# Kernel tuning notes

Hardware: AMD Instinct MI355X
Metric: run time of the kernel (lower is better)

Reference implementation:

```python
import jax, jax.numpy as jnp
import numpy as np

WH, WW = 8, 8
N = WH * WW
DIM = 128
H = 4
B_ = 8192


def _make_buffers():
    # relative_coords_table: [1, 2Wh-1, 2Ww-1, 2]
    ch = np.arange(-(WH - 1), WH, dtype=np.float32)
    cw = np.arange(-(WW - 1), WW, dtype=np.float32)
    gh, gw = np.meshgrid(ch, cw, indexing='ij')
    table = np.stack([gh, gw], axis=-1)[None]  # [1, 2Wh-1, 2Ww-1, 2]
    table[..., 0] /= (WH - 1 + 1e-12)
    table[..., 1] /= (WW - 1 + 1e-12)
    table *= 8.0
    table = np.sign(table) * np.log2(np.abs(table) + 1.0) / np.log2(8.0)
    # relative_position_index: [N, N]
    yh, yw = np.meshgrid(np.arange(WH), np.arange(WW), indexing='ij')
    coords = np.stack([yh, yw]).reshape(2, -1)  # [2, N]
    rel = coords[:, :, None] - coords[:, None, :]  # [2, N, N]
    rel = rel.transpose(1, 2, 0).astype(np.int64)
    rel[..., 0] += WH - 1
    rel[..., 1] += WW - 1
    rel[..., 0] *= 2 * WW - 1
    idx = rel.sum(-1)
    return jnp.asarray(table, jnp.float32), jnp.asarray(idx, jnp.int32)


def setup_inputs() -> dict:
    key = jax.random.key(0)
    ks = jax.random.split(key, 9)
    s = 0.02
    rel_table, rel_index = _make_buffers()
    return {
        'x': jax.random.normal(ks[0], (B_, N, DIM), jnp.float32),
        'W_qkv': jax.random.normal(ks[1], (3 * DIM, DIM), jnp.float32) * s,
        'q_bias': jax.random.normal(ks[2], (DIM,), jnp.float32) * s,
        'v_bias': jax.random.normal(ks[3], (DIM,), jnp.float32) * s,
        'logit_scale': jnp.full((H, 1, 1), jnp.log(10.0), jnp.float32),
        'cpb_w1': jax.random.normal(ks[4], (512, 2), jnp.float32) * s,
        'cpb_b1': jax.random.normal(ks[5], (512,), jnp.float32) * s,
        'cpb_w2': jax.random.normal(ks[6], (H, 512), jnp.float32) * s,
        'proj_w': jax.random.normal(ks[7], (DIM, DIM), jnp.float32) * s,
        'proj_b': jax.random.normal(ks[8], (DIM,), jnp.float32) * s,
        'rel_table': rel_table,
        'rel_index': rel_index,
    }


def reference(x, W_qkv, q_bias, v_bias, logit_scale, cpb_w1, cpb_b1, cpb_w2,
              proj_w, proj_b, rel_table, rel_index):
    B, n, C = x.shape
    hd = C // H
    # qkv projection with Swin-V2 bias layout (k bias frozen at zero)
    qkv_bias = jnp.concatenate([q_bias, jnp.zeros_like(v_bias), v_bias])
    qkv = x @ W_qkv.T + qkv_bias               # [B, N, 3C]
    qkv = qkv.reshape(B, n, 3, H, hd).transpose(2, 0, 3, 1, 4)
    q, k, v = qkv[0], qkv[1], qkv[2]           # [B, H, N, hd]
    # cosine attention
    qn = q / jnp.maximum(jnp.linalg.norm(q, axis=-1, keepdims=True), 1e-12)
    kn = k / jnp.maximum(jnp.linalg.norm(k, axis=-1, keepdims=True), 1e-12)
    attn = jnp.einsum('bhnd,bhmd->bhnm', qn, kn)
    scale = jnp.exp(jnp.minimum(logit_scale, jnp.log(1.0 / 0.01)))  # [H,1,1]
    attn = attn * scale
    # continuous position bias MLP -> gather -> 16*sigmoid
    hmid = jax.nn.relu(rel_table @ cpb_w1.T + cpb_b1)      # [1,15,15,512]
    bias_table = (hmid @ cpb_w2.T).reshape(-1, H)          # [(2Wh-1)(2Ww-1), H]
    rpb = bias_table[rel_index.reshape(-1)].reshape(n, n, H)
    rpb = 16.0 * jax.nn.sigmoid(rpb.transpose(2, 0, 1))    # [H, N, N]
    attn = jax.nn.softmax(attn + rpb[None], axis=-1)
    out = jnp.einsum('bhnm,bhmd->bhnd', attn, v)           # [B, H, N, hd]
    out = out.transpose(0, 2, 1, 3).reshape(B, n, C)
    return out @ proj_w.T + proj_b
```

## Files before the change

kernel.cpp:

```cpp
#include <hip/hip_runtime.h>

typedef short bf16x8 __attribute__((ext_vector_type(8)));
typedef float f32x4 __attribute__((ext_vector_type(4)));

__device__ __forceinline__ unsigned cvt_pk_bf16(float lo, float hi) {
  unsigned r;
  asm("v_cvt_pk_bf16_f32 %0, %1, %2" : "=v"(r) : "v"(lo), "v"(hi));
  return r;
}

__device__ __forceinline__ bf16x8 pack4(unsigned a, unsigned b, unsigned c, unsigned d) {
  union { unsigned u[4]; bf16x8 v; } t;
  t.u[0] = a; t.u[1] = b; t.u[2] = c; t.u[3] = d;
  return t.v;
}

__device__ __forceinline__ unsigned short f2bf(float f) {
  unsigned u = __float_as_uint(f);
  unsigned r = (u + 0x7fffu + ((u >> 16) & 1u)) >> 16;
  return (unsigned short)r;
}

__global__ __launch_bounds__(256) void prep(
    const float* __restrict__ W_qkv, const float* __restrict__ proj_w,
    const float* __restrict__ cpb_w1, const float* __restrict__ cpb_b1,
    const float* __restrict__ cpb_w2, const float* __restrict__ rel_table,
    const int* __restrict__ rel_index,
    bf16x8* __restrict__ wq, bf16x8* __restrict__ wp, float* __restrict__ rpbf)
{
  const int b = blockIdx.x, t = threadIdx.x;
  if (b < 32) {
    int g = b * 256 + t;
    if (g < 6144) {
      int c = g >> 8, kk = (g >> 6) & 3, l = g & 63;
      const float* s = W_qkv + (c * 16 + (l & 15)) * 128 + kk * 32 + (l >> 4) * 8;
      bf16x8 v;
      #pragma unroll
      for (int j = 0; j < 8; ++j) v[j] = (short)f2bf(s[j]);
      wq[g] = v;
    } else {
      int gl = g - 6144;
      int c = gl >> 8, kk = (gl >> 6) & 3, l = gl & 63;
      const float* row = proj_w + (c * 16 + (l & 15)) * 128;
      bf16x8 v;
      #pragma unroll
      for (int j = 0; j < 8; ++j)
        v[j] = (short)f2bf(row[kk * 32 + (j >> 2) * 16 + (l >> 4) * 4 + (j & 3)]);
      wp[gl] = v;
    }
  } else {
    __shared__ float bt[900];
    if (t < 225) {
      float t0 = rel_table[t * 2], t1 = rel_table[t * 2 + 1];
      float a0 = 0.f, a1 = 0.f, a2 = 0.f, a3 = 0.f;
      for (int j = 0; j < 512; ++j) {
        float hm = fmaxf(t0 * cpb_w1[j * 2] + t1 * cpb_w1[j * 2 + 1] + cpb_b1[j], 0.f);
        a0 += hm * cpb_w2[j];
        a1 += hm * cpb_w2[512 + j];
        a2 += hm * cpb_w2[1024 + j];
        a3 += hm * cpb_w2[1536 + j];
      }
      bt[t * 4 + 0] = a0; bt[t * 4 + 1] = a1;
      bt[t * 4 + 2] = a2; bt[t * 4 + 3] = a3;
    }
    __syncthreads();
    for (int i = t; i < 16384; i += 256) {
      int hrc = i >> 8, lane = (i >> 2) & 63, j = i & 3;
      int hh = hrc >> 4, r = (hrc >> 2) & 3, c = hrc & 3;
      int n = r * 16 + (lane & 15);
      int m = c * 16 + ((lane >> 4) << 2) + j;
      float v = bt[rel_index[n * 64 + m] * 4 + hh];
      rpbf[i] = 16.0f * __fdividef(1.0f, 1.0f + __expf(-v));
    }
  }
}

__global__ __launch_bounds__(256, 3) void win_attn(
    const float* __restrict__ x,
    const float* __restrict__ q_bias,
    const float* __restrict__ v_bias,
    const float* __restrict__ logit_scale,
    const float* __restrict__ proj_b,
    const float* __restrict__ rpbf,
    const bf16x8* __restrict__ wq,
    const bf16x8* __restrict__ wp,
    float* __restrict__ out)
{
  __shared__ __align__(128) char lds[16384];
  const int tid  = threadIdx.x;
  const int lane = tid & 63;
  const int h    = tid >> 6;
  const int l15  = lane & 15;
  const int l4   = lane >> 4;
  const int swl  = (l15 & 7) << 4;
  const long base = (long)blockIdx.x * 8192;
  const f32x4 fzero = {0.f, 0.f, 0.f, 0.f};

  {
    const float4* xp = (const float4*)(x + base);
    #pragma unroll
    for (int i = 0; i < 8; ++i) {
      float4 v = xp[i * 256 + tid];
      int e   = (i * 256 + tid) * 4;
      int row = e >> 7;
      int cb  = (e & 127) * 2;
      uint2 pk = { cvt_pk_bf16(v.x, v.y), cvt_pk_bf16(v.z, v.w) };
      *(uint2*)(lds + ((row * 256 + cb) ^ ((row & 7) << 4))) = pk;
    }
  }
  __syncthreads();

  bf16x8 aq[4], bk[4], bv[2][2];

  {
    f32x4 qT[2][4], kT[2][4];
    #pragma unroll
    for (int ct = 0; ct < 2; ++ct)
      #pragma unroll
      for (int rt = 0; rt < 4; ++rt) { qT[ct][rt] = fzero; kT[ct][rt] = fzero; }

    #pragma unroll
    for (int kk = 0; kk < 4; ++kk) {
      bf16x8 a[4];
      #pragma unroll
      for (int rt = 0; rt < 4; ++rt) {
        int row = rt * 16 + l15;
        a[rt] = *(const bf16x8*)(lds + ((row * 256 + kk * 64 + l4 * 16) ^ swl));
      }
      #pragma unroll
      for (int ct = 0; ct < 2; ++ct) {
        bf16x8 wqf = wq[((2 * h + ct) * 4 + kk) * 64 + lane];
        bf16x8 wkf = wq[((8 + 2 * h + ct) * 4 + kk) * 64 + lane];
        #pragma unroll
        for (int rt = 0; rt < 4; ++rt) {
          qT[ct][rt] = __builtin_amdgcn_mfma_f32_16x16x32_bf16(wqf, a[rt], qT[ct][rt], 0, 0, 0);
          kT[ct][rt] = __builtin_amdgcn_mfma_f32_16x16x32_bf16(wkf, a[rt], kT[ct][rt], 0, 0, 0);
        }
      }
    }

    float scale = __expf(fminf(logit_scale[h], 4.6051701859880914f));
    float4 qb0 = *(const float4*)&q_bias[h * 32 + l4 * 4];
    float4 qb1 = *(const float4*)&q_bias[h * 32 + 16 + l4 * 4];
    #pragma unroll
    for (int rt = 0; rt < 4; ++rt) {
      float tq0 = qT[0][rt][0] + qb0.x, tq1 = qT[0][rt][1] + qb0.y;
      float tq2 = qT[0][rt][2] + qb0.z, tq3 = qT[0][rt][3] + qb0.w;
      float tq4 = qT[1][rt][0] + qb1.x, tq5 = qT[1][rt][1] + qb1.y;
      float tq6 = qT[1][rt][2] + qb1.z, tq7 = qT[1][rt][3] + qb1.w;
      float sq = tq0*tq0 + tq1*tq1 + tq2*tq2 + tq3*tq3
               + tq4*tq4 + tq5*tq5 + tq6*tq6 + tq7*tq7;
      float sk = kT[0][rt][0]*kT[0][rt][0] + kT[0][rt][1]*kT[0][rt][1]
               + kT[0][rt][2]*kT[0][rt][2] + kT[0][rt][3]*kT[0][rt][3]
               + kT[1][rt][0]*kT[1][rt][0] + kT[1][rt][1]*kT[1][rt][1]
               + kT[1][rt][2]*kT[1][rt][2] + kT[1][rt][3]*kT[1][rt][3];
      sq += __shfl_xor(sq, 16); sq += __shfl_xor(sq, 32);
      sk += __shfl_xor(sk, 16); sk += __shfl_xor(sk, 32);
      float iq = __fdividef(scale, fmaxf(sqrtf(sq), 1e-12f));
      float ik = __fdividef(1.0f,  fmaxf(sqrtf(sk), 1e-12f));
      aq[rt] = pack4(cvt_pk_bf16(tq0 * iq, tq1 * iq), cvt_pk_bf16(tq2 * iq, tq3 * iq),
                     cvt_pk_bf16(tq4 * iq, tq5 * iq), cvt_pk_bf16(tq6 * iq, tq7 * iq));
      bk[rt] = pack4(cvt_pk_bf16(kT[0][rt][0] * ik, kT[0][rt][1] * ik),
                     cvt_pk_bf16(kT[0][rt][2] * ik, kT[0][rt][3] * ik),
                     cvt_pk_bf16(kT[1][rt][0] * ik, kT[1][rt][1] * ik),
                     cvt_pk_bf16(kT[1][rt][2] * ik, kT[1][rt][3] * ik));
    }
  }

  {
    f32x4 vN[2][4];
    #pragma unroll
    for (int ct = 0; ct < 2; ++ct)
      #pragma unroll
      for (int rt = 0; rt < 4; ++rt) vN[ct][rt] = fzero;

    #pragma unroll
    for (int kk = 0; kk < 4; ++kk) {
      bf16x8 a[4];
      #pragma unroll
      for (int rt = 0; rt < 4; ++rt) {
        int row = rt * 16 + l15;
        a[rt] = *(const bf16x8*)(lds + ((row * 256 + kk * 64 + l4 * 16) ^ swl));
      }
      #pragma unroll
      for (int ct = 0; ct < 2; ++ct) {
        bf16x8 wvf = wq[((16 + 2 * h + ct) * 4 + kk) * 64 + lane];
        #pragma unroll
        for (int rt = 0; rt < 4; ++rt)
          vN[ct][rt] = __builtin_amdgcn_mfma_f32_16x16x32_bf16(a[rt], wvf, vN[ct][rt], 0, 0, 0);
      }
    }
    __syncthreads();

    float vb0 = v_bias[h * 32 + l15], vb1 = v_bias[h * 32 + 16 + l15];
    #pragma unroll
    for (int ks = 0; ks < 2; ++ks)
      #pragma unroll
      for (int ct = 0; ct < 2; ++ct) {
        float vb = ct ? vb1 : vb0;
        bv[ks][ct] = pack4(
            cvt_pk_bf16(vN[ct][2 * ks][0] + vb, vN[ct][2 * ks][1] + vb),
            cvt_pk_bf16(vN[ct][2 * ks][2] + vb, vN[ct][2 * ks][3] + vb),
            cvt_pk_bf16(vN[ct][2 * ks + 1][0] + vb, vN[ct][2 * ks + 1][1] + vb),
            cvt_pk_bf16(vN[ct][2 * ks + 1][2] + vb, vN[ct][2 * ks + 1][3] + vb));
      }
  }

  {
    const f32x4* rp = (const f32x4*)rpbf;
    #pragma unroll
    for (int r = 0; r < 4; ++r) {
      f32x4 st[4];
      #pragma unroll
      for (int c = 0; c < 4; ++c)
        st[c] = __builtin_amdgcn_mfma_f32_16x16x32_bf16(
            bk[c], aq[r], rp[(h * 16 + r * 4 + c) * 64 + lane], 0, 0, 0);

      float mx = st[0][0];
      #pragma unroll
      for (int c = 0; c < 4; ++c)
        #pragma unroll
        for (int j = 0; j < 4; ++j) mx = fmaxf(mx, st[c][j]);
      mx = fmaxf(mx, __shfl_xor(mx, 16));
      mx = fmaxf(mx, __shfl_xor(mx, 32));

      float e[4][4];
      float sum = 0.f;
      #pragma unroll
      for (int c = 0; c < 4; ++c)
        #pragma unroll
        for (int j = 0; j < 4; ++j) { e[c][j] = __expf(st[c][j] - mx); sum += e[c][j]; }
      sum += __shfl_xor(sum, 16); sum += __shfl_xor(sum, 32);
      float rs = __fdividef(1.0f, sum);

      bf16x8 ap0 = pack4(cvt_pk_bf16(e[0][0], e[0][1]), cvt_pk_bf16(e[0][2], e[0][3]),
                         cvt_pk_bf16(e[1][0], e[1][1]), cvt_pk_bf16(e[1][2], e[1][3]));
      bf16x8 ap1 = pack4(cvt_pk_bf16(e[2][0], e[2][1]), cvt_pk_bf16(e[2][2], e[2][3]),
                         cvt_pk_bf16(e[3][0], e[3][1]), cvt_pk_bf16(e[3][2], e[3][3]));

      f32x4 o0 = __builtin_amdgcn_mfma_f32_16x16x32_bf16(bv[0][0], ap0, fzero, 0, 0, 0);
      o0 = __builtin_amdgcn_mfma_f32_16x16x32_bf16(bv[1][0], ap1, o0, 0, 0, 0);
      f32x4 o1 = __builtin_amdgcn_mfma_f32_16x16x32_bf16(bv[0][1], ap0, fzero, 0, 0, 0);
      o1 = __builtin_amdgcn_mfma_f32_16x16x32_bf16(bv[1][1], ap1, o1, 0, 0, 0);

      int n = r * 16 + l15;
      uint4 w = { cvt_pk_bf16(o0[0] * rs, o0[1] * rs), cvt_pk_bf16(o0[2] * rs, o0[3] * rs),
                  cvt_pk_bf16(o1[0] * rs, o1[1] * rs), cvt_pk_bf16(o1[2] * rs, o1[3] * rs) };
      *(uint4*)(lds + ((n * 256 + h * 64 + 16 * l4) ^ ((n & 7) << 4))) = w;
    }
  }
  __syncthreads();

  {
    const int n = h * 16 + l15;
    f32x4 po[8];
    #pragma unroll
    for (int c2 = 0; c2 < 8; ++c2) po[c2] = fzero;
    #pragma unroll
    for (int kk = 0; kk < 4; ++kk) {
      bf16x8 ob = *(const bf16x8*)(lds + ((n * 256 + kk * 64 + 16 * l4) ^ swl));
      #pragma unroll
      for (int c2 = 0; c2 < 8; ++c2) {
        bf16x8 wf = wp[(c2 * 4 + kk) * 64 + lane];
        po[c2] = __builtin_amdgcn_mfma_f32_16x16x32_bf16(wf, ob, po[c2], 0, 0, 0);
      }
    }
    float* op = out + base + (long)n * 128;
    #pragma unroll
    for (int c2 = 0; c2 < 8; ++c2) {
      float4 pb = *(const float4*)&proj_b[c2 * 16 + l4 * 4];
      float4 v = { po[c2][0] + pb.x, po[c2][1] + pb.y,
                   po[c2][2] + pb.z, po[c2][3] + pb.w };
      *(float4*)&op[c2 * 16 + l4 * 4] = v;
    }
  }
}

extern "C" void kernel_launch(void* const* d_in, const int* in_sizes, int n_in,
                              void* d_out, int out_size, void* d_ws, size_t ws_size,
                              hipStream_t stream) {
  (void)n_in; (void)out_size; (void)ws_size;
  const float* x           = (const float*)d_in[0];
  const float* W_qkv       = (const float*)d_in[1];
  const float* q_bias      = (const float*)d_in[2];
  const float* v_bias      = (const float*)d_in[3];
  const float* logit_scale = (const float*)d_in[4];
  const float* cpb_w1      = (const float*)d_in[5];
  const float* cpb_b1      = (const float*)d_in[6];
  const float* cpb_w2      = (const float*)d_in[7];
  const float* proj_w      = (const float*)d_in[8];
  const float* proj_b      = (const float*)d_in[9];
  const float* rel_table   = (const float*)d_in[10];
  const int*   rel_index   = (const int*)d_in[11];

  float*  rpbf = (float*)d_ws;
  bf16x8* wq   = (bf16x8*)((char*)d_ws + 65536);
  bf16x8* wp   = (bf16x8*)((char*)d_ws + 65536 + 98304);

  int nwin = in_sizes[0] / 8192;

  prep<<<33, 256, 0, stream>>>(W_qkv, proj_w, cpb_w1, cpb_b1, cpb_w2,
                               rel_table, rel_index, wq, wp, rpbf);
  win_attn<<<nwin, 256, 0, stream>>>(x, q_bias, v_bias, logit_scale, proj_b,
                                     rpbf, wq, wp, (float*)d_out);
}
```

Baseline: 246.0 us.

## Make window-attention kernel persistent over 8 windows with register prefetch of next x

Each block now processes 8 windows in a loop instead of one, prefetching the next window's x into registers during the projection epilogue and alternating between two LDS buffers. Barriers become a raw lgkmcnt wait plus s_barrier, the occupancy hint rises from 3 to 4 blocks, and output stores become nontemporal. The aim is to hide global load latency and amortise per-block launch and weight-fetch overhead. The cost is 1024 blocks instead of 8192, which may leave the GPU less balanced, plus extra register pressure from the prefetch buffer.

```diff
diff --git a/kernel.cpp b/kernel.cpp
--- a/kernel.cpp
+++ b/kernel.cpp
@@ -1,4 +1,6 @@
 #include <hip/hip_runtime.h>
+
+#define WPB 8
 
 typedef short bf16x8 __attribute__((ext_vector_type(8)));
 typedef float f32x4 __attribute__((ext_vector_type(4)));
@@ -19,6 +21,10 @@
   unsigned u = __float_as_uint(f);
   unsigned r = (u + 0x7fffu + ((u >> 16) & 1u)) >> 16;
   return (unsigned short)r;
+}
+
+__device__ __forceinline__ void bar_lds() {
+  asm volatile("s_waitcnt lgkmcnt(0)\n\ts_barrier" ::: "memory");
 }
 
 __global__ __launch_bounds__(256) void prep(
@@ -75,7 +81,7 @@
   }
 }
 
-__global__ __launch_bounds__(256, 3) void win_attn(
+__global__ __launch_bounds__(256, 4) void win_attn(
     const float* __restrict__ x,
     const float* __restrict__ q_bias,
     const float* __restrict__ v_bias,
@@ -84,194 +90,217 @@
     const float* __restrict__ rpbf,
     const bf16x8* __restrict__ wq,
     const bf16x8* __restrict__ wp,
-    float* __restrict__ out)
+    float* __restrict__ out, int nwin)
 {
-  __shared__ __align__(128) char lds[16384];
+  __shared__ __align__(128) char lds[2][16384];
   const int tid  = threadIdx.x;
   const int lane = tid & 63;
   const int h    = tid >> 6;
   const int l15  = lane & 15;
   const int l4   = lane >> 4;
   const int swl  = (l15 & 7) << 4;
-  const long base = (long)blockIdx.x * 8192;
   const f32x4 fzero = {0.f, 0.f, 0.f, 0.f};
 
+  const int w0 = blockIdx.x * WPB;
+  const int rem = nwin - w0;
+  const int nw = rem < WPB ? rem : WPB;
+
+  float4 pf[8];
   {
-    const float4* xp = (const float4*)(x + base);
+    const float4* xp = (const float4*)(x + (long)w0 * 8192);
+    #pragma unroll
+    for (int i = 0; i < 8; ++i) pf[i] = xp[i * 256 + tid];
+  }
+
+  for (int w = 0; w < nw; ++w) {
+    char* buf = lds[w & 1];
+    const long base = (long)(w0 + w) * 8192;
+
+    const bf16x8* wql = wq;                 asm("" : "+s"(wql));
+    const bf16x8* wpl = wp;                 asm("" : "+s"(wpl));
+    const f32x4*  rp  = (const f32x4*)rpbf; asm("" : "+s"(rp));
+
     #pragma unroll
     for (int i = 0; i < 8; ++i) {
-      float4 v = xp[i * 256 + tid];
+      float4 v = pf[i];
       int e   = (i * 256 + tid) * 4;
       int row = e >> 7;
       int cb  = (e & 127) * 2;
       uint2 pk = { cvt_pk_bf16(v.x, v.y), cvt_pk_bf16(v.z, v.w) };
-      *(uint2*)(lds + ((row * 256 + cb) ^ ((row & 7) << 4))) = pk;
-    }
-  }
-  __syncthreads();
-
-  bf16x8 aq[4], bk[4], bv[2][2];
-
-  {
-    f32x4 qT[2][4], kT[2][4];
-    #pragma unroll
-    for (int ct = 0; ct < 2; ++ct)
-      #pragma unroll
-      for (int rt = 0; rt < 4; ++rt) { qT[ct][rt] = fzero; kT[ct][rt] = fzero; }
-
-    #pragma unroll
-    for (int kk = 0; kk < 4; ++kk) {
-      bf16x8 a[4];
+      *(uint2*)(buf + ((row * 256 + cb) ^ ((row & 7) << 4))) = pk;
+    }
+    bar_lds();
+
+    bf16x8 aq[4], bk[4], bv[2][2];
+
+    {
+      f32x4 qT[2][4], kT[2][4];
+      #pragma unroll
+      for (int ct = 0; ct < 2; ++ct)
+        #pragma unroll
+        for (int rt = 0; rt < 4; ++rt) { qT[ct][rt] = fzero; kT[ct][rt] = fzero; }
+
+      #pragma unroll
+      for (int kk = 0; kk < 4; ++kk) {
+        bf16x8 a[4];
+        #pragma unroll
+        for (int rt = 0; rt < 4; ++rt) {
+          int row = rt * 16 + l15;
+          a[rt] = *(const bf16x8*)(buf + ((row * 256 + kk * 64 + l4 * 16) ^ swl));
+        }
+        #pragma unroll
+        for (int ct = 0; ct < 2; ++ct) {
+          bf16x8 wqf = wql[((2 * h + ct) * 4 + kk) * 64 + lane];
+          bf16x8 wkf = wql[((8 + 2 * h + ct) * 4 + kk) * 64 + lane];
+          #pragma unroll
+          for (int rt = 0; rt < 4; ++rt) {
+            qT[ct][rt] = __builtin_amdgcn_mfma_f32_16x16x32_bf16(wqf, a[rt], qT[ct][rt], 0, 0, 0);
+            kT[ct][rt] = __builtin_amdgcn_mfma_f32_16x16x32_bf16(wkf, a[rt], kT[ct][rt], 0, 0, 0);
+          }
+        }
+      }
+
+      float scale = __expf(fminf(logit_scale[h], 4.6051701859880914f));
+      float4 qb0 = *(const float4*)&q_bias[h * 32 + l4 * 4];
+      float4 qb1 = *(const float4*)&q_bias[h * 32 + 16 + l4 * 4];
       #pragma unroll
       for (int rt = 0; rt < 4; ++rt) {
-        int row = rt * 16 + l15;
-        a[rt] = *(const bf16x8*)(lds + ((row * 256 + kk * 64 + l4 * 16) ^ swl));
-      }
-      #pragma unroll
-      for (int ct = 0; ct < 2; ++ct) {
-        bf16x8 wqf = wq[((2 * h + ct) * 4 + kk) * 64 + lane];
-        bf16x8 wkf = wq[((8 + 2 * h + ct) * 4 + kk) * 64 + lane];
+        float tq0 = qT[0][rt][0] + qb0.x, tq1 = qT[0][rt][1] + qb0.y;
+        float tq2 = qT[0][rt][2] + qb0.z, tq3 = qT[0][rt][3] + qb0.w;
+        float tq4 = qT[1][rt][0] + qb1.x, tq5 = qT[1][rt][1] + qb1.y;
+        float tq6 = qT[1][rt][2] + qb1.z, tq7 = qT[1][rt][3] + qb1.w;
+        float sq = tq0*tq0 + tq1*tq1 + tq2*tq2 + tq3*tq3
+                 + tq4*tq4 + tq5*tq5 + tq6*tq6 + tq7*tq7;
+        float sk = kT[0][rt][0]*kT[0][rt][0] + kT[0][rt][1]*kT[0][rt][1]
+                 + kT[0][rt][2]*kT[0][rt][2] + kT[0][rt][3]*kT[0][rt][3]
+                 + kT[1][rt][0]*kT[1][rt][0] + kT[1][rt][1]*kT[1][rt][1]
+                 + kT[1][rt][2]*kT[1][rt][2] + kT[1][rt][3]*kT[1][rt][3];
+        sq += __shfl_xor(sq, 16); sq += __shfl_xor(sq, 32);
+        sk += __shfl_xor(sk, 16); sk += __shfl_xor(sk, 32);
+        float iq = __fdividef(scale, fmaxf(sqrtf(sq), 1e-12f));
+        float ik = __fdividef(1.0f,  fmaxf(sqrtf(sk), 1e-12f));
+        aq[rt] = pack4(cvt_pk_bf16(tq0 * iq, tq1 * iq), cvt_pk_bf16(tq2 * iq, tq3 * iq),
+                       cvt_pk_bf16(tq4 * iq, tq5 * iq), cvt_pk_bf16(tq6 * iq, tq7 * iq));
+        bk[rt] = pack4(cvt_pk_bf16(kT[0][rt][0] * ik, kT[0][rt][1] * ik),
+                       cvt_pk_bf16(kT[0][rt][2] * ik, kT[0][rt][3] * ik),
+                       cvt_pk_bf16(kT[1][rt][0] * ik, kT[1][rt][1] * ik),
+                       cvt_pk_bf16(kT[1][rt][2] * ik, kT[1][rt][3] * ik));
+      }
+    }
+
+    {
+      f32x4 vN[2][4];
+      #pragma unroll
+      for (int ct = 0; ct < 2; ++ct)
+        #pragma unroll
+        for (int rt = 0; rt < 4; ++rt) vN[ct][rt] = fzero;
+
+      #pragma unroll
+      for (int kk = 0; kk < 4; ++kk) {
+        bf16x8 a[4];
         #pragma unroll
         for (int rt = 0; rt < 4; ++rt) {
-          qT[ct][rt] = __builtin_amdgcn_mfma_f32_16x16x32_bf16(wqf, a[rt], qT[ct][rt], 0, 0, 0);
-          kT[ct][rt] = __builtin_amdgcn_mfma_f32_16x16x32_bf16(wkf, a[rt], kT[ct][rt], 0, 0, 0);
-        }
-      }
-    }
-
-    float scale = __expf(fminf(logit_scale[h], 4.6051701859880914f));
-    float4 qb0 = *(const float4*)&q_bias[h * 32 + l4 * 4];
-    float4 qb1 = *(const float4*)&q_bias[h * 32 + 16 + l4 * 4];
-    #pragma unroll
-    for (int rt = 0; rt < 4; ++rt) {
-      float tq0 = qT[0][rt][0] + qb0.x, tq1 = qT[0][rt][1] + qb0.y;
-      float tq2 = qT[0][rt][2] + qb0.z, tq3 = qT[0][rt][3] + qb0.w;
-      float tq4 = qT[1][rt][0] + qb1.x, tq5 = qT[1][rt][1] + qb1.y;
-      float tq6 = qT[1][rt][2] + qb1.z, tq7 = qT[1][rt][3] + qb1.w;
-      float sq = tq0*tq0 + tq1*tq1 + tq2*tq2 + tq3*tq3
-               + tq4*tq4 + tq5*tq5 + tq6*tq6 + tq7*tq7;
-      float sk = kT[0][rt][0]*kT[0][rt][0] + kT[0][rt][1]*kT[0][rt][1]
-               + kT[0][rt][2]*kT[0][rt][2] + kT[0][rt][3]*kT[0][rt][3]
-               + kT[1][rt][0]*kT[1][rt][0] + kT[1][rt][1]*kT[1][rt][1]
-               + kT[1][rt][2]*kT[1][rt][2] + kT[1][rt][3]*kT[1][rt][3];
-      sq += __shfl_xor(sq, 16); sq += __shfl_xor(sq, 32);
-      sk += __shfl_xor(sk, 16); sk += __shfl_xor(sk, 32);
-      float iq = __fdividef(scale, fmaxf(sqrtf(sq), 1e-12f));
-      float ik = __fdividef(1.0f,  fmaxf(sqrtf(sk), 1e-12f));
-      aq[rt] = pack4(cvt_pk_bf16(tq0 * iq, tq1 * iq), cvt_pk_bf16(tq2 * iq, tq3 * iq),
-                     cvt_pk_bf16(tq4 * iq, tq5 * iq), cvt_pk_bf16(tq6 * iq, tq7 * iq));
-      bk[rt] = pack4(cvt_pk_bf16(kT[0][rt][0] * ik, kT[0][rt][1] * ik),
-                     cvt_pk_bf16(kT[0][rt][2] * ik, kT[0][rt][3] * ik),
-                     cvt_pk_bf16(kT[1][rt][0] * ik, kT[1][rt][1] * ik),
-                     cvt_pk_bf16(kT[1][rt][2] * ik, kT[1][rt][3] * ik));
-    }
-  }
-
-  {
-    f32x4 vN[2][4];
-    #pragma unroll
-    for (int ct = 0; ct < 2; ++ct)
-      #pragma unroll
-      for (int rt = 0; rt < 4; ++rt) vN[ct][rt] = fzero;
-
-    #pragma unroll
-    for (int kk = 0; kk < 4; ++kk) {
-      bf16x8 a[4];
-      #pragma unroll
-      for (int rt = 0; rt < 4; ++rt) {
-        int row = rt * 16 + l15;
-        a[rt] = *(const bf16x8*)(lds + ((row * 256 + kk * 64 + l4 * 16) ^ swl));
-      }
-      #pragma unroll
-      for (int ct = 0; ct < 2; ++ct) {
-        bf16x8 wvf = wq[((16 + 2 * h + ct) * 4 + kk) * 64 + lane];
-        #pragma unroll
-        for (int rt = 0; rt < 4; ++rt)
-          vN[ct][rt] = __builtin_amdgcn_mfma_f32_16x16x32_bf16(a[rt], wvf, vN[ct][rt], 0, 0, 0);
-      }
-    }
-    __syncthreads();
-
-    float vb0 = v_bias[h * 32 + l15], vb1 = v_bias[h * 32 + 16 + l15];
-    #pragma unroll
-    for (int ks = 0; ks < 2; ++ks)
-      #pragma unroll
-      for (int ct = 0; ct < 2; ++ct) {
-        float vb = ct ? vb1 : vb0;
-        bv[ks][ct] = pack4(
-            cvt_pk_bf16(vN[ct][2 * ks][0] + vb, vN[ct][2 * ks][1] + vb),
-            cvt_pk_bf16(vN[ct][2 * ks][2] + vb, vN[ct][2 * ks][3] + vb),
-            cvt_pk_bf16(vN[ct][2 * ks + 1][0] + vb, vN[ct][2 * ks + 1][1] + vb),
-            cvt_pk_bf16(vN[ct][2 * ks + 1][2] + vb, vN[ct][2 * ks + 1][3] + vb));
-      }
-  }
-
-  {
-    const f32x4* rp = (const f32x4*)rpbf;
-    #pragma unroll
-    for (int r = 0; r < 4; ++r) {
-      f32x4 st[4];
-      #pragma unroll
-      for (int c = 0; c < 4; ++c)
-        st[c] = __builtin_amdgcn_mfma_f32_16x16x32_bf16(
-            bk[c], aq[r], rp[(h * 16 + r * 4 + c) * 64 + lane], 0, 0, 0);
-
-      float mx = st[0][0];
-      #pragma unroll
-      for (int c = 0; c < 4; ++c)
-        #pragma unroll
-        for (int j = 0; j < 4; ++j) mx = fmaxf(mx, st[c][j]);
-      mx = fmaxf(mx, __shfl_xor(mx, 16));
-      mx = fmaxf(mx, __shfl_xor(mx, 32));
-
-      float e[4][4];
-      float sum = 0.f;
-      #pragma unroll
-      for (int c = 0; c < 4; ++c)
-        #pragma unroll
-        for (int j = 0; j < 4; ++j) { e[c][j] = __expf(st[c][j] - mx); sum += e[c][j]; }
-      sum += __shfl_xor(sum, 16); sum += __shfl_xor(sum, 32);
-      float rs = __fdividef(1.0f, sum);
-
-      bf16x8 ap0 = pack4(cvt_pk_bf16(e[0][0], e[0][1]), cvt_pk_bf16(e[0][2], e[0][3]),
-                         cvt_pk_bf16(e[1][0], e[1][1]), cvt_pk_bf16(e[1][2], e[1][3]));
-      bf16x8 ap1 = pack4(cvt_pk_bf16(e[2][0], e[2][1]), cvt_pk_bf16(e[2][2], e[2][3]),
-                         cvt_pk_bf16(e[3][0], e[3][1]), cvt_pk_bf16(e[3][2], e[3][3]));
-
-      f32x4 o0 = __builtin_amdgcn_mfma_f32_16x16x32_bf16(bv[0][0], ap0, fzero, 0, 0, 0);
-      o0 = __builtin_amdgcn_mfma_f32_16x16x32_bf16(bv[1][0], ap1, o0, 0, 0, 0);
-      f32x4 o1 = __builtin_amdgcn_mfma_f32_16x16x32_bf16(bv[0][1], ap0, fzero, 0, 0, 0);
-      o1 = __builtin_amdgcn_mfma_f32_16x16x32_bf16(bv[1][1], ap1, o1, 0, 0, 0);
-
-      int n = r * 16 + l15;
-      uint4 w = { cvt_pk_bf16(o0[0] * rs, o0[1] * rs), cvt_pk_bf16(o0[2] * rs, o0[3] * rs),
-                  cvt_pk_bf16(o1[0] * rs, o1[1] * rs), cvt_pk_bf16(o1[2] * rs, o1[3] * rs) };
-      *(uint4*)(lds + ((n * 256 + h * 64 + 16 * l4) ^ ((n & 7) << 4))) = w;
-    }
-  }
-  __syncthreads();
-
-  {
-    const int n = h * 16 + l15;
-    f32x4 po[8];
-    #pragma unroll
-    for (int c2 = 0; c2 < 8; ++c2) po[c2] = fzero;
-    #pragma unroll
-    for (int kk = 0; kk < 4; ++kk) {
-      bf16x8 ob = *(const bf16x8*)(lds + ((n * 256 + kk * 64 + 16 * l4) ^ swl));
+          int row = rt * 16 + l15;
+          a[rt] = *(const bf16x8*)(buf + ((row * 256 + kk * 64 + l4 * 16) ^ swl));
+        }
+        #pragma unroll
+        for (int ct = 0; ct < 2; ++ct) {
+          bf16x8 wvf = wql[((16 + 2 * h + ct) * 4 + kk) * 64 + lane];
+          #pragma unroll
+          for (int rt = 0; rt < 4; ++rt)
+            vN[ct][rt] = __builtin_amdgcn_mfma_f32_16x16x32_bf16(a[rt], wvf, vN[ct][rt], 0, 0, 0);
+        }
+      }
+      bar_lds();
+
+      float vb0 = v_bias[h * 32 + l15], vb1 = v_bias[h * 32 + 16 + l15];
+      #pragma unroll
+      for (int ks = 0; ks < 2; ++ks)
+        #pragma unroll
+        for (int ct = 0; ct < 2; ++ct) {
+          float vb = ct ? vb1 : vb0;
+          bv[ks][ct] = pack4(
+              cvt_pk_bf16(vN[ct][2 * ks][0] + vb, vN[ct][2 * ks][1] + vb),
+              cvt_pk_bf16(vN[ct][2 * ks][2] + vb, vN[ct][2 * ks][3] + vb),
+              cvt_pk_bf16(vN[ct][2 * ks + 1][0] + vb, vN[ct][2 * ks + 1][1] + vb),
+              cvt_pk_bf16(vN[ct][2 * ks + 1][2] + vb, vN[ct][2 * ks + 1][3] + vb));
+        }
+    }
+
+    {
+      #pragma unroll
+      for (int r = 0; r < 4; ++r) {
+        f32x4 st[4];
+        #pragma unroll
+        for (int c = 0; c < 4; ++c)
+          st[c] = __builtin_amdgcn_mfma_f32_16x16x32_bf16(
+              bk[c], aq[r], rp[(h * 16 + r * 4 + c) * 64 + lane], 0, 0, 0);
+
+        float mx = st[0][0];
+        #pragma unroll
+        for (int c = 0; c < 4; ++c)
+          #pragma unroll
+          for (int j = 0; j < 4; ++j) mx = fmaxf(mx, st[c][j]);
+        mx = fmaxf(mx, __shfl_xor(mx, 16));
+        mx = fmaxf(mx, __shfl_xor(mx, 32));
+
+        float e[4][4];
+        float sum = 0.f;
+        #pragma unroll
+        for (int c = 0; c < 4; ++c)
+          #pragma unroll
+          for (int j = 0; j < 4; ++j) { e[c][j] = __expf(st[c][j] - mx); sum += e[c][j]; }
+        sum += __shfl_xor(sum, 16); sum += __shfl_xor(sum, 32);
+        float rs = __fdividef(1.0f, sum);
+
+        bf16x8 ap0 = pack4(cvt_pk_bf16(e[0][0], e[0][1]), cvt_pk_bf16(e[0][2], e[0][3]),
+                           cvt_pk_bf16(e[1][0], e[1][1]), cvt_pk_bf16(e[1][2], e[1][3]));
+        bf16x8 ap1 = pack4(cvt_pk_bf16(e[2][0], e[2][1]), cvt_pk_bf16(e[2][2], e[2][3]),
+                           cvt_pk_bf16(e[3][0], e[3][1]), cvt_pk_bf16(e[3][2], e[3][3]));
+
+        f32x4 o0 = __builtin_amdgcn_mfma_f32_16x16x32_bf16(bv[0][0], ap0, fzero, 0, 0, 0);
+        o0 = __builtin_amdgcn_mfma_f32_16x16x32_bf16(bv[1][0], ap1, o0, 0, 0, 0);
+        f32x4 o1 = __builtin_amdgcn_mfma_f32_16x16x32_bf16(bv[0][1], ap0, fzero, 0, 0, 0);
+        o1 = __builtin_amdgcn_mfma_f32_16x16x32_bf16(bv[1][1], ap1, o1, 0, 0, 0);
+
+        int n = r * 16 + l15;
+        uint4 wv4 = { cvt_pk_bf16(o0[0] * rs, o0[1] * rs), cvt_pk_bf16(o0[2] * rs, o0[3] * rs),
+                      cvt_pk_bf16(o1[0] * rs, o1[1] * rs), cvt_pk_bf16(o1[2] * rs, o1[3] * rs) };
+        *(uint4*)(buf + ((n * 256 + h * 64 + 16 * l4) ^ ((n & 7) << 4))) = wv4;
+      }
+    }
+    bar_lds();
+
+    {
+      const int n = h * 16 + l15;
+      f32x4 po[8];
+      #pragma unroll
+      for (int c2 = 0; c2 < 8; ++c2) po[c2] = fzero;
+      #pragma unroll
+      for (int kk = 0; kk < 4; ++kk) {
+        bf16x8 ob = *(const bf16x8*)(buf + ((n * 256 + kk * 64 + 16 * l4) ^ swl));
+        #pragma unroll
+        for (int c2 = 0; c2 < 8; ++c2) {
+          bf16x8 wf = wpl[(c2 * 4 + kk) * 64 + lane];
+          po[c2] = __builtin_amdgcn_mfma_f32_16x16x32_bf16(wf, ob, po[c2], 0, 0, 0);
+        }
+      }
+
+      __builtin_amdgcn_sched_barrier(0);
+      if (w + 1 < nw) {
+        const float4* xp = (const float4*)(x + base + 8192);
+        #pragma unroll
+        for (int i = 0; i < 8; ++i) pf[i] = xp[i * 256 + tid];
+      }
+
+      float* op = out + base + (long)n * 128;
       #pragma unroll
       for (int c2 = 0; c2 < 8; ++c2) {
-        bf16x8 wf = wp[(c2 * 4 + kk) * 64 + lane];
-        po[c2] = __builtin_amdgcn_mfma_f32_16x16x32_bf16(wf, ob, po[c2], 0, 0, 0);
-      }
-    }
-    float* op = out + base + (long)n * 128;
-    #pragma unroll
-    for (int c2 = 0; c2 < 8; ++c2) {
-      float4 pb = *(const float4*)&proj_b[c2 * 16 + l4 * 4];
-      float4 v = { po[c2][0] + pb.x, po[c2][1] + pb.y,
-                   po[c2][2] + pb.z, po[c2][3] + pb.w };
-      *(float4*)&op[c2 * 16 + l4 * 4] = v;
+        float4 pb = *(const float4*)&proj_b[c2 * 16 + l4 * 4];
+        f32x4 v = { po[c2][0] + pb.x, po[c2][1] + pb.y,
+                    po[c2][2] + pb.z, po[c2][3] + pb.w };
+        __builtin_nontemporal_store(v, (f32x4*)&op[c2 * 16 + l4 * 4]);
+      }
     }
   }
 }
@@ -298,9 +327,10 @@
   bf16x8* wp   = (bf16x8*)((char*)d_ws + 65536 + 98304);
 
   int nwin = in_sizes[0] / 8192;
+  int nblk = (nwin + WPB - 1) / WPB;
 
   prep<<<33, 256, 0, stream>>>(W_qkv, proj_w, cpb_w1, cpb_b1, cpb_w2,
                                rel_table, rel_index, wq, wp, rpbf);
-  win_attn<<<nwin, 256, 0, stream>>>(x, q_bias, v_bias, logit_scale, proj_b,
-                                     rpbf, wq, wp, (float*)d_out);
-}
+  win_attn<<<nblk, 256, 0, stream>>>(x, q_bias, v_bias, logit_scale, proj_b,
+                                     rpbf, wq, wp, (float*)d_out, nwin);
+}
```

Result: slower. 781.1 us (+217.5%).
